# Kernel tuning notes

Measured on AMD Instinct MI355X. Metric: run time of the kernel, lower is better.

The kernel has to match this reference:

```python
import jax, jax.numpy as jnp
import numpy as np

N, C, E, S = 16384, 128, 262144, 10
AVG_NUM_NEIGHBORS = 16.0
INV_SQRT3 = 1.0 / np.sqrt(3.0)


def setup_inputs() -> dict:
    key = jax.random.key(0)
    ks = jax.random.split(key, 15)
    return dict(
        node_specie=jax.random.randint(ks[0], (N,), 0, S),
        node_feats=jax.random.normal(ks[1], (N, C, 4), jnp.float32),   # irreps 0e+1o per channel
        edge_attrs=jax.random.normal(ks[2], (E, 4), jnp.float32),      # Y: 0e+1o
        edge_feats=jax.random.normal(ks[3], (E, 8), jnp.float32),      # radial scalars
        senders=jax.random.randint(ks[4], (E,), 0, N),
        receivers=jax.random.randint(ks[5], (E,), 0, N),
        W_sc0=jax.random.normal(ks[6], (S, C, C), jnp.float32),
        W_sc1=jax.random.normal(ks[7], (S, C, C), jnp.float32),
        W_pre0=jax.random.normal(ks[8], (C, C), jnp.float32),
        W_pre1=jax.random.normal(ks[9], (C, C), jnp.float32),
        W_mlp1=jax.random.normal(ks[10], (8, 64), jnp.float32),
        W_mlp2=jax.random.normal(ks[11], (64, 64), jnp.float32),
        W_mlp3=jax.random.normal(ks[12], (64, 4), jnp.float32),
        W_post0=jax.random.normal(ks[13], (C, 2, C), jnp.float32),
        W_post1=jax.random.normal(ks[14], (C, 2, C), jnp.float32),
    )


def reference(node_specie, node_feats, edge_attrs, edge_feats, senders, receivers,
              W_sc0, W_sc1, W_pre0, W_pre1, W_mlp1, W_mlp2, W_mlp3, W_post0, W_post1):
    inv_c = 1.0 / np.sqrt(C)
    s_in = node_feats[..., 0]      # [N,C] 0e
    v_in = node_feats[..., 1:4]    # [N,C,3] 1o

    # linear_sc: per-species equivariant linear (0e+1o -> hidden 0e+1o)
    sc_s = jnp.einsum('nc,ncd->nd', s_in, W_sc0[node_specie]) * inv_c
    sc_v = jnp.einsum('nci,ncd->ndi', v_in, W_sc1[node_specie]) * inv_c
    sc = jnp.concatenate([sc_s[..., None], sc_v], axis=-1)  # [N,C,4]

    # linear_premp: channel-mixing equivariant linear (same irreps)
    s = (s_in @ W_pre0) * inv_c                              # [N,C]
    v = jnp.einsum('nci,cd->ndi', v_in, W_pre1) * inv_c      # [N,C,3]

    # MessagePassingConvolution (channel axis kept instead of hk.vmap)
    se_s = s[senders]              # [E,C]
    se_v = v[senders]              # [E,C,3]
    a = edge_attrs[:, 1:4]         # drop 0e part of Y -> 1o
    dot = jnp.einsum('eci,ei->ec', se_v, a) * INV_SQRT3      # 1o x 1o -> 0e
    sva = se_s[..., None] * a[:, None, :]                    # 0e x 1o -> 1o

    # radial MLP -> one mixing scalar per irrep (num_irreps = 4), shared across channels
    h = jax.nn.silu((edge_feats @ W_mlp1) * (1.0 / np.sqrt(8.0)))
    h = jax.nn.silu((h @ W_mlp2) * 0.125)
    mix = (h @ W_mlp3) * 0.125                               # [E,4]

    # messages irreps 2x0e+2x1o: [s, dot | v, s*a], each block scaled by its mix scalar
    msg = jnp.concatenate([
        se_s[..., None] * mix[:, None, 0:1],
        dot[..., None] * mix[:, None, 1:2],
        se_v * mix[:, None, 2:3],
        sva * mix[:, None, 3:4],
    ], axis=-1)                                              # [E,C,8]

    agg = jnp.zeros((N, C, 8), msg.dtype).at[receivers].add(msg) / AVG_NUM_NEIGHBORS

    # linear_postmp: (2x0e+2x1o, C channels) -> (0e+1o, C channels)
    inv2c = 1.0 / np.sqrt(2 * C)
    o_s = jnp.einsum('ncm,cmd->nd', agg[..., :2], W_post0) * inv2c
    o_v = jnp.einsum('ncmi,cmd->ndi', agg[..., 2:].reshape(N, C, 2, 3), W_post1) * inv2c
    node_out = jnp.concatenate([o_s[..., None], o_v], axis=-1)  # [N,C,4]
    return node_out, sc
```

## Files before the change

### kernel.cpp

```cpp
#include <hip/hip_runtime.h>
#include <hip/hip_bf16.h>

#define N_NODES 16384
#define C_DIM   128
#define E_EDGES 262144
#define S_SPEC  10
#define CHUNK   256
#define PROWS   16544
#define PTILES  1034

__device__ __constant__ const float INV_C  = 0.08838834764831845f;
__device__ __constant__ const float INV_2C = 0.0625f;
#define F_INV_SQRT3 0.5773502691896258f
#define F_INV_SQRT8 0.35355339059327373f
#define F_INV_AVG   0.0625f

typedef __attribute__((ext_vector_type(8))) short bf16x8;
typedef __attribute__((ext_vector_type(4))) float f32x4;

__device__ __forceinline__ float silu(float x) {
    return x / (1.0f + __expf(-x));
}

__device__ __forceinline__ unsigned short f2bf(float x) {
    __hip_bfloat16 h = __float2bfloat16(x);
    return *reinterpret_cast<unsigned short*>(&h);
}

__device__ __forceinline__ unsigned int pack2bf(float lo, float hi) {
    return (unsigned int)f2bf(lo) | ((unsigned int)f2bf(hi) << 16);
}

__device__ __forceinline__ float bf2f(unsigned int u16) {
    return __uint_as_float((u16 & 0xffffu) << 16);
}

__device__ __forceinline__ float bf2f_hi(unsigned int u) {
    return __uint_as_float(u & 0xffff0000u);
}

__global__ __launch_bounds__(256) void init_kernel(
    int* __restrict__ counts, int* __restrict__ scnt,
    int* __restrict__ prow_map, int* __restrict__ tile_spec)
{
    const int idx = blockIdx.x * 256 + threadIdx.x;
    if (idx < N_NODES) counts[idx] = 0;
    if (idx < S_SPEC)  scnt[idx] = 0;
    if (idx < PROWS)   prow_map[idx] = -1;
    if (idx < PTILES)  tile_spec[idx] = 0;
}

__global__ __launch_bounds__(256) void hist_kernel(
    const int* __restrict__ receivers, int* __restrict__ cnt,
    const int* __restrict__ specie, int* __restrict__ scnt)
{
    __shared__ int h[S_SPEC];
    const int t = threadIdx.x;
    const bool doSpec = blockIdx.x < (N_NODES / 256);
    if (doSpec) {
        if (t < S_SPEC) h[t] = 0;
        __syncthreads();
        atomicAdd(&h[specie[blockIdx.x * 256 + t]], 1);
    }
    const int e = blockIdx.x * 256 + t;
    atomicAdd(&cnt[receivers[e]], 1);
    if (doSpec) {
        __syncthreads();
        if (t < S_SPEC) atomicAdd(&scnt[t], h[t]);
    }
}

__global__ __launch_bounds__(256) void scan_kernel(
    const int* __restrict__ cnt, int* __restrict__ start,
    int* __restrict__ cursor,
    const int* __restrict__ scnt, int* __restrict__ poff,
    int* __restrict__ scur)
{
    __shared__ int sums[256];
    const int t = threadIdx.x;
    if (t == 0) {
        int pa = 0;
        for (int i = 0; i < S_SPEC; ++i) {
            poff[i] = pa;
            scur[i] = 0;
            pa += ((scnt[i] + 15) >> 4) << 4;
        }
    }
    int s = 0;
    for (int i = 0; i < 64; ++i) s += cnt[t * 64 + i];
    sums[t] = s;
    __syncthreads();
    if (t == 0) {
        int a = 0;
        for (int i = 0; i < 256; ++i) { int v = sums[i]; sums[i] = a; a += v; }
    }
    __syncthreads();
    int a = sums[t];
    for (int i = 0; i < 64; ++i) {
        int v = cnt[t * 64 + i];
        start[t * 64 + i] = a;
        cursor[t * 64 + i] = a;
        a += v;
    }
    if (t == 255) start[N_NODES] = a;
}

__global__ __launch_bounds__(256) void scatter_place_kernel(
    const int* __restrict__ receivers, int* __restrict__ cursor,
    int* __restrict__ perm,
    const int* __restrict__ specie, const int* __restrict__ poff,
    int* __restrict__ scur,
    int* __restrict__ prow_map, int* __restrict__ tile_spec)
{
    const int t = threadIdx.x;
    const int e = blockIdx.x * 256 + t;
    const int pos = atomicAdd(&cursor[receivers[e]], 1);
    perm[pos] = e;

    if (blockIdx.x < (N_NODES / 256)) {
        __shared__ int h[S_SPEC];
        __shared__ int bbase[S_SPEC];
        if (t < S_SPEC) h[t] = 0;
        __syncthreads();
        const int n = blockIdx.x * 256 + t;
        const int s = specie[n];
        const int lrank = atomicAdd(&h[s], 1);
        __syncthreads();
        if (t < S_SPEC && h[t] > 0) bbase[t] = atomicAdd(&scur[t], h[t]);
        __syncthreads();
        const int p = poff[s] + bbase[s] + lrank;
        prow_map[p] = n;
        tile_spec[p >> 4] = s;
    }
}

__global__ __launch_bounds__(256) void prep_kernel(
    const int* __restrict__ prow_map, const float* __restrict__ node_feats,
    ushort* __restrict__ As, ushort* __restrict__ Av0,
    ushort* __restrict__ Av1, ushort* __restrict__ Av2,
    const float* __restrict__ Wsc0, const float* __restrict__ Wsc1,
    ushort* __restrict__ Wsc0t, ushort* __restrict__ Wsc1t,
    const float* __restrict__ Wpre0, const float* __restrict__ Wpre1,
    ushort* __restrict__ Wpre0t, ushort* __restrict__ Wpre1t,
    const float* __restrict__ Wp0, const float* __restrict__ Wp1,
    ushort* __restrict__ Bt0, ushort* __restrict__ Bt1,
    const float* __restrict__ Wm1, const float* __restrict__ Wm2,
    const float* __restrict__ Wm3,
    ushort* __restrict__ W1t, ushort* __restrict__ W2t,
    ushort* __restrict__ W3t)
{
    const int idx = blockIdx.x * 256 + threadIdx.x;
    {
        const int p = idx >> 7, c = idx & 127;
        const int nid = prow_map[p];
        float4 f = {0.0f, 0.0f, 0.0f, 0.0f};
        if (nid >= 0) f = ((const float4*)node_feats)[nid * C_DIM + c];
        As [idx] = f2bf(f.x);
        Av0[idx] = f2bf(f.y);
        Av1[idx] = f2bf(f.z);
        Av2[idx] = f2bf(f.w);
    }
    if (idx < S_SPEC * 128 * 128) {
        const int s = idx >> 14, d = (idx >> 7) & 127, k = idx & 127;
        Wsc0t[idx] = f2bf(Wsc0[s * 16384 + k * 128 + d] * INV_C);
        Wsc1t[idx] = f2bf(Wsc1[s * 16384 + k * 128 + d] * INV_C);
    }
    if (idx < 16384) {
        const int d = idx >> 7, k = idx & 127;
        Wpre0t[idx] = f2bf(Wpre0[k * 128 + d] * INV_C);
        Wpre1t[idx] = f2bf(Wpre1[k * 128 + d] * INV_C);
    }
    if (idx < 32768) {
        const int k = idx >> 7, d = idx & 127;
        Bt0[d * 256 + k] = f2bf(Wp0[idx] * INV_2C);
        Bt1[d * 256 + k] = f2bf(Wp1[idx] * INV_2C);
    }
    if (idx < 4096) {
        if (idx < 2048) {
            const int hh = idx >> 5, k = idx & 31;
            W1t[idx] = (k < 8) ? f2bf(Wm1[k * 64 + hh] * F_INV_SQRT8) : (ushort)0;
        }
        {
            const int c = idx >> 6, k = idx & 63;
            W2t[idx] = f2bf(Wm2[k * 64 + c] * 0.125f);
        }
        if (idx < 1024) {
            const int m = idx >> 6, k = idx & 63;
            W3t[idx] = (m < 4) ? f2bf(Wm3[k * 4 + m] * 0.125f) : (ushort)0;
        }
    }
}

__global__ __launch_bounds__(512) void node_gemm_kernel(
    const int* __restrict__ prow_map,
    const int* __restrict__ tile_spec,
    const ushort* __restrict__ As,
    const ushort* __restrict__ Av0,
    const ushort* __restrict__ Av1,
    const ushort* __restrict__ Av2,
    const ushort* __restrict__ Wsc0t,
    const ushort* __restrict__ Wsc1t,
    const ushort* __restrict__ Wpre0t,
    const ushort* __restrict__ Wpre1t,
    float* __restrict__ out_sc,
    ushort4* __restrict__ sv_bf)
{
    const int l  = threadIdx.x & 63;
    const int w  = threadIdx.x >> 6;
    const int d0 = w * 16;
    const int lr = l & 15;
    const int lg = l >> 4;

    bf16x8 bp0[4], bp1[4];
#pragma unroll
    for (int ks = 0; ks < 4; ++ks) {
        bp0[ks] = *reinterpret_cast<const bf16x8*>(
            Wpre0t + (d0 + lr) * 128 + ks * 32 + lg * 8);
        bp1[ks] = *reinterpret_cast<const bf16x8*>(
            Wpre1t + (d0 + lr) * 128 + ks * 32 + lg * 8);
    }

    const int tile = blockIdx.x;
    const int sp   = tile_spec[tile];
    const int r0   = tile * 16;

    const ushort* as  = As  + (size_t)(r0 + lr) * 128 + lg * 8;
    const ushort* av0 = Av0 + (size_t)(r0 + lr) * 128 + lg * 8;
    const ushort* av1 = Av1 + (size_t)(r0 + lr) * 128 + lg * 8;
    const ushort* av2 = Av2 + (size_t)(r0 + lr) * 128 + lg * 8;
    const ushort* ws0 = Wsc0t + (size_t)sp * 16384 + (d0 + lr) * 128 + lg * 8;
    const ushort* ws1 = Wsc1t + (size_t)sp * 16384 + (d0 + lr) * 128 + lg * 8;

    const f32x4 zero = {0.0f, 0.0f, 0.0f, 0.0f};
    f32x4 aS0 = zero, aS1 = zero, aS2 = zero, aS3 = zero;
    f32x4 aP0 = zero, aP1 = zero, aP2 = zero, aP3 = zero;

#pragma unroll
    for (int ks = 0; ks < 4; ++ks) {
        const bf16x8 a_s  = *reinterpret_cast<const bf16x8*>(as  + ks * 32);
        const bf16x8 a_v0 = *reinterpret_cast<const bf16x8*>(av0 + ks * 32);
        const bf16x8 a_v1 = *reinterpret_cast<const bf16x8*>(av1 + ks * 32);
        const bf16x8 a_v2 = *reinterpret_cast<const bf16x8*>(av2 + ks * 32);
        const bf16x8 bs0  = *reinterpret_cast<const bf16x8*>(ws0 + ks * 32);
        const bf16x8 bs1  = *reinterpret_cast<const bf16x8*>(ws1 + ks * 32);
        aS0 = __builtin_amdgcn_mfma_f32_16x16x32_bf16(a_s,  bs0, aS0, 0, 0, 0);
        aS1 = __builtin_amdgcn_mfma_f32_16x16x32_bf16(a_v0, bs1, aS1, 0, 0, 0);
        aS2 = __builtin_amdgcn_mfma_f32_16x16x32_bf16(a_v1, bs1, aS2, 0, 0, 0);
        aS3 = __builtin_amdgcn_mfma_f32_16x16x32_bf16(a_v2, bs1, aS3, 0, 0, 0);
        aP0 = __builtin_amdgcn_mfma_f32_16x16x32_bf16(a_s,  bp0[ks], aP0, 0, 0, 0);
        aP1 = __builtin_amdgcn_mfma_f32_16x16x32_bf16(a_v0, bp1[ks], aP1, 0, 0, 0);
        aP2 = __builtin_amdgcn_mfma_f32_16x16x32_bf16(a_v1, bp1[ks], aP2, 0, 0, 0);
        aP3 = __builtin_amdgcn_mfma_f32_16x16x32_bf16(a_v2, bp1[ks], aP3, 0, 0, 0);
    }

#pragma unroll
    for (int r = 0; r < 4; ++r) {
        const int row = r0 + lg * 4 + r;
        const int nid = prow_map[row];
        if (nid >= 0) {
            float4 o = {aS0[r], aS1[r], aS2[r], aS3[r]};
            ((float4*)out_sc)[(size_t)nid * C_DIM + (d0 + lr)] = o;
            ushort4 pv = {f2bf(aP0[r]), f2bf(aP1[r]), f2bf(aP2[r]), f2bf(aP3[r])};
            sv_bf[(size_t)nid * C_DIM + (d0 + lr)] = pv;
        }
    }
}

__global__ __launch_bounds__(256) void edge_mlp_mfma_kernel(
    const float* __restrict__ edge_feats,
    const float* __restrict__ edge_attrs,
    const ushort* __restrict__ W1t,
    const ushort* __restrict__ W2t,
    const ushort* __restrict__ W3t,
    uint4* __restrict__ coefbf)
{
    __shared__ ushort h_lds[4][16][72];

    const int w  = threadIdx.x >> 6;
    const int l  = threadIdx.x & 63;
    const int lr = l & 15;
    const int lg = l >> 4;

    bf16x8 a1[4];
#pragma unroll
    for (int mt = 0; mt < 4; ++mt)
        a1[mt] = *reinterpret_cast<const bf16x8*>(
            W1t + (mt * 16 + lr) * 32 + lg * 8);
    bf16x8 a2[4][2];
#pragma unroll
    for (int mt = 0; mt < 4; ++mt)
#pragma unroll
        for (int ks = 0; ks < 2; ++ks)
            a2[mt][ks] = *reinterpret_cast<const bf16x8*>(
                W2t + (mt * 16 + lr) * 64 + ks * 32 + lg * 8);
    bf16x8 a3[2];
#pragma unroll
    for (int ks = 0; ks < 2; ++ks)
        a3[ks] = *reinterpret_cast<const bf16x8*>(
            W3t + lr * 64 + ks * 32 + lg * 8);

    const int tile = blockIdx.x * 4 + w;
    const int e0   = tile * 16;
    const f32x4 zero = {0.0f, 0.0f, 0.0f, 0.0f};

    bf16x8 b1 = {0, 0, 0, 0, 0, 0, 0, 0};
    if (lg == 0) {
        const float4 q0 = *(const float4*)(edge_feats + (size_t)(e0 + lr) * 8);
        const float4 q1 = *(const float4*)(edge_feats + (size_t)(e0 + lr) * 8 + 4);
        b1[0] = (short)f2bf(q0.x); b1[1] = (short)f2bf(q0.y);
        b1[2] = (short)f2bf(q0.z); b1[3] = (short)f2bf(q0.w);
        b1[4] = (short)f2bf(q1.x); b1[5] = (short)f2bf(q1.y);
        b1[6] = (short)f2bf(q1.z); b1[7] = (short)f2bf(q1.w);
    }

    f32x4 d1[4];
#pragma unroll
    for (int mt = 0; mt < 4; ++mt)
        d1[mt] = __builtin_amdgcn_mfma_f32_16x16x32_bf16(a1[mt], b1, zero, 0, 0, 0);

#pragma unroll
    for (int mt = 0; mt < 4; ++mt) {
        uint2 p;
        p.x = pack2bf(silu(d1[mt][0]), silu(d1[mt][1]));
        p.y = pack2bf(silu(d1[mt][2]), silu(d1[mt][3]));
        *reinterpret_cast<uint2*>(&h_lds[w][lr][mt * 16 + lg * 4]) = p;
    }
    __syncthreads();

    bf16x8 b2[2];
#pragma unroll
    for (int ks = 0; ks < 2; ++ks)
        b2[ks] = *reinterpret_cast<const bf16x8*>(
            &h_lds[w][lr][ks * 32 + lg * 8]);

    f32x4 d2[4];
#pragma unroll
    for (int mt = 0; mt < 4; ++mt) {
        d2[mt] = __builtin_amdgcn_mfma_f32_16x16x32_bf16(a2[mt][0], b2[0], zero, 0, 0, 0);
        d2[mt] = __builtin_amdgcn_mfma_f32_16x16x32_bf16(a2[mt][1], b2[1], d2[mt], 0, 0, 0);
    }

#pragma unroll
    for (int mt = 0; mt < 4; ++mt) {
        uint2 p;
        p.x = pack2bf(silu(d2[mt][0]), silu(d2[mt][1]));
        p.y = pack2bf(silu(d2[mt][2]), silu(d2[mt][3]));
        *reinterpret_cast<uint2*>(&h_lds[w][lr][mt * 16 + lg * 4]) = p;
    }
    __syncthreads();

    bf16x8 b3[2];
#pragma unroll
    for (int ks = 0; ks < 2; ++ks)
        b3[ks] = *reinterpret_cast<const bf16x8*>(
            &h_lds[w][lr][ks * 32 + lg * 8]);

    f32x4 d3;
    d3 = __builtin_amdgcn_mfma_f32_16x16x32_bf16(a3[0], b3[0], zero, 0, 0, 0);
    d3 = __builtin_amdgcn_mfma_f32_16x16x32_bf16(a3[1], b3[1], d3, 0, 0, 0);

    if (lg == 0) {
        const int e = e0 + lr;
        const float4 a = *(const float4*)(edge_attrs + (size_t)e * 4);
        const float mx0 = d3[0], mx1 = d3[1], mx2 = d3[2], mx3 = d3[3];
        uint4 cv;
        cv.x = pack2bf(mx0,                      mx1 * a.y * F_INV_SQRT3);
        cv.y = pack2bf(mx1 * a.z * F_INV_SQRT3,  mx1 * a.w * F_INV_SQRT3);
        cv.z = pack2bf(mx2,                      mx3 * a.y);
        cv.w = pack2bf(mx3 * a.z,                mx3 * a.w);
        coefbf[e] = cv;
    }
}

__global__ __launch_bounds__(256) void agg_kernel(
    const int* __restrict__ start,
    const int* __restrict__ perm,
    const int* __restrict__ senders,
    const uint4* __restrict__ coefbf,
    const ushort4* __restrict__ sv_bf,
    unsigned int* __restrict__ A_s,
    unsigned int* __restrict__ A_v)
{
    __shared__ int   se_lds[CHUNK];
    __shared__ float sc_lds[CHUNK][8];

    const int n0   = blockIdx.x * 8;
    const int t    = threadIdx.x;
    const int c    = t & 127;
    const int half = t >> 7;

    int nbeg[4], nend[4];
#pragma unroll
    for (int k = 0; k < 4; ++k) {
        nbeg[k] = start[n0 + half * 4 + k];
        nend[k] = start[n0 + half * 4 + k + 1];
    }

    const int blk_beg = start[n0];
    const int blk_end = start[n0 + 8];

    float acc[4][8] = {};

    for (int cb = blk_beg; cb < blk_end; cb += CHUNK) {
        const int cn = min(CHUNK, blk_end - cb);
        __syncthreads();
        for (int j = t; j < cn; j += 256) {
            const int e = perm[cb + j];
            se_lds[j] = senders[e];
            const uint4 cv = coefbf[e];
            float4 lo = {bf2f(cv.x), bf2f_hi(cv.x), bf2f(cv.y), bf2f_hi(cv.y)};
            float4 hi = {bf2f(cv.z), bf2f_hi(cv.z), bf2f(cv.w), bf2f_hi(cv.w)};
            ((float4*)sc_lds[j])[0] = lo;
            ((float4*)sc_lds[j])[1] = hi;
        }
        __syncthreads();

#pragma unroll
        for (int k = 0; k < 4; ++k) {
            const int lo = max(nbeg[k], cb);
            const int hi = min(nend[k], cb + cn);
            int idx = lo;
            for (; idx + 2 <= hi; idx += 2) {
                const int j0 = idx - cb, j1 = j0 + 1;
                const int snd0 = se_lds[j0];
                const int snd1 = se_lds[j1];
                const ushort4 u0 = sv_bf[(size_t)snd0 * C_DIM + c];
                const ushort4 u1 = sv_bf[(size_t)snd1 * C_DIM + c];
                const float* kf0 = sc_lds[j0];
                const float* kf1 = sc_lds[j1];
                const float x0 = bf2f(u0.x), y0 = bf2f(u0.y),
                            z0 = bf2f(u0.z), w0 = bf2f(u0.w);
                const float x1 = bf2f(u1.x), y1 = bf2f(u1.y),
                            z1 = bf2f(u1.z), w1 = bf2f(u1.w);
                acc[k][0] += x0 * kf0[0];
                acc[k][1] += y0 * kf0[1] + z0 * kf0[2] + w0 * kf0[3];
                acc[k][2] += y0 * kf0[4];
                acc[k][3] += z0 * kf0[4];
                acc[k][4] += w0 * kf0[4];
                acc[k][5] += x0 * kf0[5];
                acc[k][6] += x0 * kf0[6];
                acc[k][7] += x0 * kf0[7];
                acc[k][0] += x1 * kf1[0];
                acc[k][1] += y1 * kf1[1] + z1 * kf1[2] + w1 * kf1[3];
                acc[k][2] += y1 * kf1[4];
                acc[k][3] += z1 * kf1[4];
                acc[k][4] += w1 * kf1[4];
                acc[k][5] += x1 * kf1[5];
                acc[k][6] += x1 * kf1[6];
                acc[k][7] += x1 * kf1[7];
            }
            if (idx < hi) {
                const int j = idx - cb;
                const int snd = se_lds[j];
                const ushort4 u = sv_bf[(size_t)snd * C_DIM + c];
                const float* kf = sc_lds[j];
                const float x = bf2f(u.x), y = bf2f(u.y),
                            z = bf2f(u.z), w = bf2f(u.w);
                acc[k][0] += x * kf[0];
                acc[k][1] += y * kf[1] + z * kf[2] + w * kf[3];
                acc[k][2] += y * kf[4];
                acc[k][3] += z * kf[4];
                acc[k][4] += w * kf[4];
                acc[k][5] += x * kf[5];
                acc[k][6] += x * kf[6];
                acc[k][7] += x * kf[7];
            }
        }
    }

#pragma unroll
    for (int k = 0; k < 4; ++k) {
        const int n = n0 + half * 4 + k;
        A_s[(size_t)n * 128 + c] =
            pack2bf(acc[k][0] * F_INV_AVG, acc[k][1] * F_INV_AVG);
        A_v[((size_t)n * 3 + 0) * 128 + c] =
            pack2bf(acc[k][2] * F_INV_AVG, acc[k][5] * F_INV_AVG);
        A_v[((size_t)n * 3 + 1) * 128 + c] =
            pack2bf(acc[k][3] * F_INV_AVG, acc[k][6] * F_INV_AVG);
        A_v[((size_t)n * 3 + 2) * 128 + c] =
            pack2bf(acc[k][4] * F_INV_AVG, acc[k][7] * F_INV_AVG);
    }
}

__global__ __launch_bounds__(512) void post_gemm_kernel(
    const ushort* __restrict__ A_s,
    const ushort* __restrict__ A_v,
    const ushort* __restrict__ Bt0,
    const ushort* __restrict__ Bt1,
    float* __restrict__ out)
{
    const int l  = threadIdx.x & 63;
    const int w  = threadIdx.x >> 6;
    const int d0 = w * 16;
    const int lr = l & 15;
    const int lg = l >> 4;

    const bool isS = blockIdx.x < 512;
    const ushort* A  = isS ? A_s : A_v;
    const ushort* Bt = isS ? Bt0 : Bt1;
    const int ntiles  = isS ? (N_NODES / 16) : (3 * N_NODES / 16);
    const int b0      = isS ? blockIdx.x : blockIdx.x - 512;
    const int gstride = isS ? 512 : 1024;

    bf16x8 bfrag[8];
#pragma unroll
    for (int ks = 0; ks < 8; ++ks) {
        bfrag[ks] = *reinterpret_cast<const bf16x8*>(
            Bt + (size_t)(d0 + lr) * 256 + ks * 32 + lg * 8);
    }

    for (int tile = b0; tile < ntiles; tile += gstride) {
        const int r0 = tile * 16;
        f32x4 acc = {0.0f, 0.0f, 0.0f, 0.0f};
        const ushort* ap = A + (size_t)(r0 + lr) * 256 + lg * 8;
#pragma unroll
        for (int ks = 0; ks < 8; ++ks) {
            bf16x8 a = *reinterpret_cast<const bf16x8*>(ap + ks * 32);
            acc = __builtin_amdgcn_mfma_f32_16x16x32_bf16(a, bfrag[ks], acc,
                                                          0, 0, 0);
        }
#pragma unroll
        for (int r = 0; r < 4; ++r) {
            const int row = r0 + lg * 4 + r;
            int n, comp;
            if (isS) { n = row; comp = 0; }
            else { n = row / 3; comp = 1 + (row - n * 3); }
            out[(size_t)n * 512 + (d0 + lr) * 4 + comp] = acc[r];
        }
    }
}

extern "C" void kernel_launch(void* const* d_in, const int* in_sizes, int n_in,
                              void* d_out, int out_size, void* d_ws, size_t ws_size,
                              hipStream_t stream)
{
    const int*   specie     = (const int*)d_in[0];
    const float* node_feats = (const float*)d_in[1];
    const float* edge_attrs = (const float*)d_in[2];
    const float* edge_feats = (const float*)d_in[3];
    const int*   senders    = (const int*)d_in[4];
    const int*   receivers  = (const int*)d_in[5];
    const float* Wsc0  = (const float*)d_in[6];
    const float* Wsc1  = (const float*)d_in[7];
    const float* Wpre0 = (const float*)d_in[8];
    const float* Wpre1 = (const float*)d_in[9];
    const float* Wm1   = (const float*)d_in[10];
    const float* Wm2   = (const float*)d_in[11];
    const float* Wm3   = (const float*)d_in[12];
    const float* Wp0   = (const float*)d_in[13];
    const float* Wp1   = (const float*)d_in[14];

    float* out_node = (float*)d_out;
    float* out_sc   = out_node + (size_t)N_NODES * C_DIM * 4;

    char* ws = (char*)d_ws;
    ushort4*      sv_bf = (ushort4*)ws;
    unsigned int* A_s   = (unsigned int*)(ws + (size_t)16 * 1024 * 1024);
    unsigned int* A_v   = A_s + (size_t)N_NODES * 128;
    uint4*        coefbf= (uint4*)(A_v + (size_t)3 * N_NODES * 128);
    ushort*       Asin  = (ushort*)(coefbf + (size_t)E_EDGES);
    ushort*       Av0in = Asin  + (size_t)PROWS * 128;
    ushort*       Av1in = Av0in + (size_t)PROWS * 128;
    ushort*       Av2in = Av1in + (size_t)PROWS * 128;
    ushort*       Bt0   = Av2in + (size_t)PROWS * 128;
    ushort*       Bt1   = Bt0 + 256 * 128;
    ushort*       Wsc0t = Bt1 + 256 * 128;
    ushort*       Wsc1t = Wsc0t + S_SPEC * 128 * 128;
    ushort*       Wpre0t = Wsc1t + S_SPEC * 128 * 128;
    ushort*       Wpre1t = Wpre0t + 128 * 128;
    ushort*       W1t   = Wpre1t + 128 * 128;
    ushort*       W2t   = W1t + 64 * 32;
    ushort*       W3t   = W2t + 64 * 64;
    int* counts    = (int*)(W3t + 16 * 64);
    int* start     = counts + N_NODES;
    int* cursor    = start + (N_NODES + 1);
    int* perm      = cursor + N_NODES;
    int* scnt      = perm + E_EDGES;
    int* poff      = scnt + S_SPEC;
    int* scur      = poff + S_SPEC;
    int* prow_map  = scur + S_SPEC;
    int* tile_spec = prow_map + PROWS;

    init_kernel<<<(PROWS + 255) / 256, 256, 0, stream>>>(
        counts, scnt, prow_map, tile_spec);

    hist_kernel<<<E_EDGES / 256, 256, 0, stream>>>(
        receivers, counts, specie, scnt);

    scan_kernel<<<1, 256, 0, stream>>>(counts, start, cursor, scnt, poff, scur);

    scatter_place_kernel<<<E_EDGES / 256, 256, 0, stream>>>(
        receivers, cursor, perm, specie, poff, scur, prow_map, tile_spec);

    prep_kernel<<<PROWS * 128 / 256, 256, 0, stream>>>(
        prow_map, node_feats, Asin, Av0in, Av1in, Av2in,
        Wsc0, Wsc1, Wsc0t, Wsc1t, Wpre0, Wpre1, Wpre0t, Wpre1t,
        Wp0, Wp1, Bt0, Bt1, Wm1, Wm2, Wm3, W1t, W2t, W3t);

    node_gemm_kernel<<<PTILES, 512, 0, stream>>>(
        prow_map, tile_spec, Asin, Av0in, Av1in, Av2in,
        Wsc0t, Wsc1t, Wpre0t, Wpre1t, out_sc, sv_bf);

    edge_mlp_mfma_kernel<<<E_EDGES / 64, 256, 0, stream>>>(
        edge_feats, edge_attrs, W1t, W2t, W3t, coefbf);

    agg_kernel<<<N_NODES / 8, 256, 0, stream>>>(
        start, perm, senders, coefbf, sv_bf, A_s, A_v);

    post_gemm_kernel<<<1536, 512, 0, stream>>>(
        (const ushort*)A_s, (const ushort*)A_v, Bt0, Bt1, out_node);
}
```

Measured before the change: 228.0 us.

## Store vector aggregates component-major and fuse post GEMM into float4 stores

The aggregation kernel now writes the vector aggregate planes component-major, one plane of N rows per spatial component, instead of interleaved per node. The post-mixing GEMM then gives each block 16 nodes and computes the scalar output and all three vector outputs together. Each lane writes its four results as one float4, replacing four strided scalar stores. This removes the division by three and the scattered writes, at the cost of more registers per thread (two sets of B fragments and four accumulators) and fewer, larger blocks.

```diff
diff --git a/kernel.cpp b/kernel.cpp
--- a/kernel.cpp
+++ b/kernel.cpp
@@ -473,11 +473,11 @@
         const int n = n0 + half * 4 + k;
         A_s[(size_t)n * 128 + c] =
             pack2bf(acc[k][0] * F_INV_AVG, acc[k][1] * F_INV_AVG);
-        A_v[((size_t)n * 3 + 0) * 128 + c] =
+        A_v[((size_t)0 * N_NODES + n) * 128 + c] =
             pack2bf(acc[k][2] * F_INV_AVG, acc[k][5] * F_INV_AVG);
-        A_v[((size_t)n * 3 + 1) * 128 + c] =
+        A_v[((size_t)1 * N_NODES + n) * 128 + c] =
             pack2bf(acc[k][3] * F_INV_AVG, acc[k][6] * F_INV_AVG);
-        A_v[((size_t)n * 3 + 2) * 128 + c] =
+        A_v[((size_t)2 * N_NODES + n) * 128 + c] =
             pack2bf(acc[k][4] * F_INV_AVG, acc[k][7] * F_INV_AVG);
     }
 }
@@ -487,7 +487,7 @@
     const ushort* __restrict__ A_v,
     const ushort* __restrict__ Bt0,
     const ushort* __restrict__ Bt1,
-    float* __restrict__ out)
+    float4* __restrict__ out)
 {
     const int l  = threadIdx.x & 63;
     const int w  = threadIdx.x >> 6;
@@ -495,38 +495,41 @@
     const int lr = l & 15;
     const int lg = l >> 4;
 
-    const bool isS = blockIdx.x < 512;
-    const ushort* A  = isS ? A_s : A_v;
-    const ushort* Bt = isS ? Bt0 : Bt1;
-    const int ntiles  = isS ? (N_NODES / 16) : (3 * N_NODES / 16);
-    const int b0      = isS ? blockIdx.x : blockIdx.x - 512;
-    const int gstride = isS ? 512 : 1024;
-
-    bf16x8 bfrag[8];
+    bf16x8 b0frag[8], b1frag[8];
 #pragma unroll
     for (int ks = 0; ks < 8; ++ks) {
-        bfrag[ks] = *reinterpret_cast<const bf16x8*>(
-            Bt + (size_t)(d0 + lr) * 256 + ks * 32 + lg * 8);
-    }
-
-    for (int tile = b0; tile < ntiles; tile += gstride) {
-        const int r0 = tile * 16;
-        f32x4 acc = {0.0f, 0.0f, 0.0f, 0.0f};
-        const ushort* ap = A + (size_t)(r0 + lr) * 256 + lg * 8;
-#pragma unroll
-        for (int ks = 0; ks < 8; ++ks) {
-            bf16x8 a = *reinterpret_cast<const bf16x8*>(ap + ks * 32);
-            acc = __builtin_amdgcn_mfma_f32_16x16x32_bf16(a, bfrag[ks], acc,
-                                                          0, 0, 0);
-        }
-#pragma unroll
-        for (int r = 0; r < 4; ++r) {
-            const int row = r0 + lg * 4 + r;
-            int n, comp;
-            if (isS) { n = row; comp = 0; }
-            else { n = row / 3; comp = 1 + (row - n * 3); }
-            out[(size_t)n * 512 + (d0 + lr) * 4 + comp] = acc[r];
-        }
+        b0frag[ks] = *reinterpret_cast<const bf16x8*>(
+            Bt0 + (size_t)(d0 + lr) * 256 + ks * 32 + lg * 8);
+        b1frag[ks] = *reinterpret_cast<const bf16x8*>(
+            Bt1 + (size_t)(d0 + lr) * 256 + ks * 32 + lg * 8);
+    }
+
+    const int r0 = blockIdx.x * 16;
+    const f32x4 zero = {0.0f, 0.0f, 0.0f, 0.0f};
+    f32x4 accS = zero, acc0 = zero, acc1 = zero, acc2 = zero;
+
+    const ushort* aS = A_s + (size_t)(r0 + lr) * 256 + lg * 8;
+    const ushort* a0 = A_v + ((size_t)0 * N_NODES + r0 + lr) * 256 + lg * 8;
+    const ushort* a1 = A_v + ((size_t)1 * N_NODES + r0 + lr) * 256 + lg * 8;
+    const ushort* a2 = A_v + ((size_t)2 * N_NODES + r0 + lr) * 256 + lg * 8;
+
+#pragma unroll
+    for (int ks = 0; ks < 8; ++ks) {
+        const bf16x8 fS = *reinterpret_cast<const bf16x8*>(aS + ks * 32);
+        const bf16x8 f0 = *reinterpret_cast<const bf16x8*>(a0 + ks * 32);
+        const bf16x8 f1 = *reinterpret_cast<const bf16x8*>(a1 + ks * 32);
+        const bf16x8 f2 = *reinterpret_cast<const bf16x8*>(a2 + ks * 32);
+        accS = __builtin_amdgcn_mfma_f32_16x16x32_bf16(fS, b0frag[ks], accS, 0, 0, 0);
+        acc0 = __builtin_amdgcn_mfma_f32_16x16x32_bf16(f0, b1frag[ks], acc0, 0, 0, 0);
+        acc1 = __builtin_amdgcn_mfma_f32_16x16x32_bf16(f1, b1frag[ks], acc1, 0, 0, 0);
+        acc2 = __builtin_amdgcn_mfma_f32_16x16x32_bf16(f2, b1frag[ks], acc2, 0, 0, 0);
+    }
+
+#pragma unroll
+    for (int r = 0; r < 4; ++r) {
+        const int n = r0 + lg * 4 + r;
+        float4 o = {accS[r], acc0[r], acc1[r], acc2[r]};
+        out[(size_t)n * C_DIM + (d0 + lr)] = o;
     }
 }
 
@@ -607,6 +610,6 @@
     agg_kernel<<<N_NODES / 8, 256, 0, stream>>>(
         start, perm, senders, coefbf, sv_bf, A_s, A_v);
 
-    post_gemm_kernel<<<1536, 512, 0, stream>>>(
-        (const ushort*)A_s, (const ushort*)A_v, Bt0, Bt1, out_node);
-}
+    post_gemm_kernel<<<N_NODES / 16, 512, 0, stream>>>(
+        (const ushort*)A_s, (const ushort*)A_v, Bt0, Bt1, (float4*)out_node);
+}
```

Measured after the change: 228.2 us. Within noise of the previous version (+0.1%).
